# Optimization experiments

Hardware: AMD Instinct MI355X
Metric: run time of the kernel (lower is better)

Reference implementation:

```python
import jax, jax.numpy as jnp
import numpy as np

E = 4
K = 2
BN_EPS = 1e-3


def _silu(y):
    return y * jax.nn.sigmoid(y)


def _bn_silu_nchw(y, g, b, m, v):
    # eval-mode BatchNorm2d over channel axis of [B, C, H, W], then SiLU
    scale = (g / jnp.sqrt(v + BN_EPS))[None, :, None, None]
    shift = (b - m * g / jnp.sqrt(v + BN_EPS))[None, :, None, None]
    return _silu(y * scale + shift)


def setup_inputs() -> dict:
    key = jax.random.key(0)
    ks = jax.random.split(key, 20)
    B, C1, C2, H, W = 32, 256, 256, 80, 80
    c_ = C2 // 2  # 128
    s = 0.05
    return {
        "x": jax.random.normal(ks[0], (B, C1, H, W), jnp.float32),
        "w1": jax.random.normal(ks[1], (c_, C1), jnp.float32) * s,
        "bn1_g": jax.random.uniform(ks[2], (c_,), jnp.float32, 0.5, 1.5),
        "bn1_b": jax.random.normal(ks[3], (c_,), jnp.float32) * s,
        "bn1_m": jax.random.normal(ks[4], (c_,), jnp.float32) * s,
        "bn1_v": jax.random.uniform(ks[5], (c_,), jnp.float32, 0.5, 1.5),
        "router_w": jax.random.normal(ks[6], (E, c_), jnp.float32) * s,
        "router_b": jax.random.normal(ks[7], (E,), jnp.float32) * s,
        "ew": jax.random.normal(ks[8], (E, c_, c_, 3, 3), jnp.float32) * s,
        "ebn_g": jax.random.uniform(ks[9], (E, c_), jnp.float32, 0.5, 1.5),
        "ebn_b": jax.random.normal(ks[10], (E, c_), jnp.float32) * s,
        "ebn_m": jax.random.normal(ks[11], (E, c_), jnp.float32) * s,
        "ebn_v": jax.random.uniform(ks[12], (E, c_), jnp.float32, 0.5, 1.5),
        "w3": jax.random.normal(ks[13], (C2, c_), jnp.float32) * s,
        "bn3_g": jax.random.uniform(ks[14], (C2,), jnp.float32, 0.5, 1.5),
        "bn3_b": jax.random.normal(ks[15], (C2,), jnp.float32) * s,
        "bn3_m": jax.random.normal(ks[16], (C2,), jnp.float32) * s,
        "bn3_v": jax.random.uniform(ks[17], (C2,), jnp.float32, 0.5, 1.5),
    }


def reference(x, w1, bn1_g, bn1_b, bn1_m, bn1_v, router_w, router_b,
              ew, ebn_g, ebn_b, ebn_m, ebn_v, w3, bn3_g, bn3_b, bn3_m, bn3_v):
    B, C1, H, W = x.shape
    c_ = w1.shape[0]

    # conv1: 1x1 conv + BN + SiLU -> [B, c_, H, W]
    x_in = _bn_silu_nchw(jnp.einsum('bchw,oc->bohw', x, w1), bn1_g, bn1_b, bn1_m, bn1_v)

    # flatten pixels to tokens [N, c_] (N = B*H*W), matching permute(0,2,3,1).reshape
    tokens = x_in.transpose(0, 2, 3, 1).reshape(-1, c_)
    N = tokens.shape[0]

    # router: 1x1 conv with bias -> per-token logits [N, E]
    logits = tokens @ router_w.T + router_b
    probs = jax.nn.softmax(logits, axis=-1)

    topw, topi = jax.lax.top_k(probs, K)                  # [N, K]
    topw = topw / jnp.sum(topw, axis=-1, keepdims=True)

    # dense [N, E] combine weights: normalized top-k weight where selected, else 0
    wd = jnp.zeros((N, E), tokens.dtype).at[jnp.arange(N)[:, None], topi].set(topw)

    # experts: 3x3 conv applied to 1x1 patches with pad=1 -> only center tap matters
    center = ew[:, :, :, 1, 1]                            # [E, c_out, c_in]
    ye = jnp.einsum('nc,eoc->neo', tokens, center)        # [N, E, c_]
    inv = ebn_g / jnp.sqrt(ebn_v + BN_EPS)                # [E, c_]
    ye = _silu(ye * inv[None] + (ebn_b - ebn_m * inv)[None])

    out_moe = jnp.einsum('neo,ne->no', ye, wd)            # weighted scatter-add
    out_moe = out_moe.reshape(B, H, W, c_).transpose(0, 3, 1, 2)

    # conv3: 1x1 conv + BN + SiLU -> [B, C2, H, W]
    x_out = _bn_silu_nchw(jnp.einsum('bchw,oc->bohw', out_moe, w3), bn3_g, bn3_b, bn3_m, bn3_v)

    # shortcut (c1 == c2 here)
    return x_out + x
```

## Files before the change

### kernel.cpp

```cpp
#include <hip/hip_runtime.h>
#include <cstdint>
#include <cstddef>

#define NEXP 4
#define CH   128
#define C1   256
#define C2   256
#define HWSZ 6400
#define NTOKS 204800
#define BNE  1e-3f

using f32x4 = __attribute__((ext_vector_type(4))) float;
using f16x8 = __attribute__((ext_vector_type(8))) _Float16;
using s16x8 = __attribute__((ext_vector_type(8))) short;

static __device__ __forceinline__ unsigned short f2bf(float f) {
    union { float f; unsigned u; } v; v.f = f;
    unsigned r = v.u + 0x7fffu + ((v.u >> 16) & 1u);
    return (unsigned short)(r >> 16);
}
static __device__ __forceinline__ f32x4 zero4() {
    f32x4 z; z[0] = 0.f; z[1] = 0.f; z[2] = 0.f; z[3] = 0.f; return z;
}

#define ASWZ(row) ((((row) >> 1) & 3) << 3)

__global__ __launch_bounds__(256) void k0_pack(const float* __restrict__ ew,
                                               const float* __restrict__ w1,
                                               const float* __restrict__ w3,
                                               unsigned short* __restrict__ cen,
                                               _Float16* __restrict__ w1s,
                                               unsigned short* __restrict__ w3p) {
    int bid = blockIdx.x;
    int tid = threadIdx.x;
    if (bid < 256) {
        int idx = bid * 256 + tid;
        cen[idx] = f2bf(ew[(size_t)idx * 9 + 4]);
    } else if (bid < 384) {
        int lin = (bid - 256) * 256 + tid;
        int o = lin >> 8, k = lin & 255;
        int s = k >> 5, kk = k & 31;
        int kks = kk ^ ASWZ(o);
        float v = w1[o * C1 + k];
        _Float16 h = (_Float16)v;
        w1s[((s * 2 + 0) * 128 + o) * 32 + kks] = h;
        w1s[((s * 2 + 1) * 128 + o) * 32 + kks] = (_Float16)((v - (float)h) * 2048.0f);
    } else {
        int lin = (bid - 384) * 256 + tid;
        int o = lin >> 7, k = lin & 127;
        int s = k >> 5, kk = k & 31;
        int kks = kk ^ ASWZ(o);
        w3p[(s * 256 + o) * 32 + kks] = f2bf(w3[o * CH + k]);
    }
}

__global__ __launch_bounds__(256, 4) void k1_conv1_router(
    const float* __restrict__ x, const _Float16* __restrict__ w1s,
    const float* __restrict__ bn1_g, const float* __restrict__ bn1_b,
    const float* __restrict__ bn1_m, const float* __restrict__ bn1_v,
    const float* __restrict__ rw, const float* __restrict__ rb,
    unsigned short* __restrict__ tokens, float* __restrict__ wd)
{
    const int tid  = threadIdx.x;
    const int lane = tid & 63;
    const int n15  = lane & 15;
    const int quad = lane >> 4;
    const int wv   = tid >> 6;

    const int nt0 = blockIdx.x * 64;
    const int b   = nt0 / HWSZ;
    const int hw0 = nt0 % HWSZ;

    __shared__ union {
        struct { _Float16 Bh[64 * 72]; _Float16 Bl[64 * 72]; } s;
        struct { float tok[64 * 132]; float logit[64 * 4]; } e;
    } u;
    __shared__ float s1_l[128], t1_l[128];

    if (tid < 128) {
        float s = bn1_g[tid] / sqrtf(bn1_v[tid] + BNE);
        s1_l[tid] = s;
        t1_l[tid] = bn1_b[tid] - bn1_m[tid] * s;
    }

    f32x4 acc_m[2][4], acc_c[2][4];
    #pragma unroll
    for (int i = 0; i < 2; i++)
        #pragma unroll
        for (int j = 0; j < 4; j++) { acc_m[i][j] = zero4(); acc_c[i][j] = zero4(); }

    for (int S = 0; S < 4; S++) {
        {
            int i  = tid & 63;
            int kg = tid >> 6;
            #pragma unroll
            for (int r = 0; r < 4; r++) {
                int k4 = kg * 16 + r * 4;
                const float* xp = x + ((size_t)(b * C1 + S * 64 + k4)) * HWSZ + hw0 + i;
                float v0 = xp[0], v1 = xp[HWSZ], v2 = xp[2 * HWSZ], v3 = xp[3 * HWSZ];
                _Float16* bh = &u.s.Bh[i * 72 + k4];
                _Float16* bl = &u.s.Bl[i * 72 + k4];
                _Float16 h0 = (_Float16)v0, h1 = (_Float16)v1, h2 = (_Float16)v2, h3 = (_Float16)v3;
                bh[0] = h0; bh[1] = h1; bh[2] = h2; bh[3] = h3;
                bl[0] = (_Float16)((v0 - (float)h0) * 2048.0f);
                bl[1] = (_Float16)((v1 - (float)h1) * 2048.0f);
                bl[2] = (_Float16)((v2 - (float)h2) * 2048.0f);
                bl[3] = (_Float16)((v3 - (float)h3) * 2048.0f);
            }
        }
        __syncthreads();

        #pragma unroll
        for (int kh = 0; kh < 2; kh++) {
            const int sl = S * 2 + kh;
            f16x8 a_h[2], a_l[2];
            #pragma unroll
            for (int mt = 0; mt < 2; mt++) {
                int row = (wv * 2 + mt) * 16 + n15;
                int col = (quad * 8) ^ ASWZ(row);
                a_h[mt] = *(const f16x8*)&w1s[((sl * 2 + 0) * 128 + row) * 32 + col];
                a_l[mt] = *(const f16x8*)&w1s[((sl * 2 + 1) * 128 + row) * 32 + col];
            }
            #pragma unroll
            for (int nt = 0; nt < 4; nt++) {
                int row = nt * 16 + n15;
                f16x8 b_h = *(const f16x8*)&u.s.Bh[row * 72 + kh * 32 + quad * 8];
                f16x8 b_l = *(const f16x8*)&u.s.Bl[row * 72 + kh * 32 + quad * 8];
                #pragma unroll
                for (int mt = 0; mt < 2; mt++) {
                    acc_m[mt][nt] = __builtin_amdgcn_mfma_f32_16x16x32_f16(a_h[mt], b_h, acc_m[mt][nt], 0, 0, 0);
                    acc_c[mt][nt] = __builtin_amdgcn_mfma_f32_16x16x32_f16(a_l[mt], b_h, acc_c[mt][nt], 0, 0, 0);
                    acc_c[mt][nt] = __builtin_amdgcn_mfma_f32_16x16x32_f16(a_h[mt], b_l, acc_c[mt][nt], 0, 0, 0);
                }
            }
        }
        __syncthreads();
    }

    #pragma unroll
    for (int mt = 0; mt < 2; mt++)
        #pragma unroll
        for (int nt = 0; nt < 4; nt++)
            #pragma unroll
            for (int r = 0; r < 4; r++) {
                int o  = (wv * 2 + mt) * 16 + quad * 4 + r;
                int tk = nt * 16 + n15;
                float y1 = acc_m[mt][nt][r] + acc_c[mt][nt][r] * (1.0f / 2048.0f);
                float y  = y1 * s1_l[o] + t1_l[o];
                u.e.tok[tk * 132 + o] = y / (1.0f + __expf(-y));
            }
    __syncthreads();

    {
        int tk = tid >> 2;
        int e  = tid & 3;
        const float* trow = &u.e.tok[tk * 132];
        const float* wrow = &rw[e * CH];
        float a0 = 0.f, a1 = 0.f, a2 = 0.f, a3 = 0.f;
        #pragma unroll 8
        for (int c = 0; c < CH; c += 4) {
            a0 = fmaf(trow[c + 0], wrow[c + 0], a0);
            a1 = fmaf(trow[c + 1], wrow[c + 1], a1);
            a2 = fmaf(trow[c + 2], wrow[c + 2], a2);
            a3 = fmaf(trow[c + 3], wrow[c + 3], a3);
        }
        u.e.logit[tk * 4 + e] = ((a0 + a1) + (a2 + a3)) + rb[e];
    }
    __syncthreads();

    if (tid < 64) {
        const float* lg = &u.e.logit[tid * 4];
        float l0 = lg[0], l1 = lg[1], l2 = lg[2], l3 = lg[3];
        int i1 = 0; float m1 = l0;
        if (l1 > m1) { m1 = l1; i1 = 1; }
        if (l2 > m1) { m1 = l2; i1 = 2; }
        if (l3 > m1) { m1 = l3; i1 = 3; }
        int i2 = -1; float m2 = -3.4e38f;
        if (i1 != 0 && l0 > m2) { m2 = l0; i2 = 0; }
        if (i1 != 1 && l1 > m2) { m2 = l1; i2 = 1; }
        if (i1 != 2 && l2 > m2) { m2 = l2; i2 = 2; }
        if (i1 != 3 && l3 > m2) { m2 = l3; i2 = 3; }
        float p2 = __expf(m2 - m1);
        float wa = 1.0f / (1.0f + p2);
        float wb = p2 * wa;
        float4 wout;
        wout.x = (i1 == 0) ? wa : ((i2 == 0) ? wb : 0.0f);
        wout.y = (i1 == 1) ? wa : ((i2 == 1) ? wb : 0.0f);
        wout.z = (i1 == 2) ? wa : ((i2 == 2) ? wb : 0.0f);
        wout.w = (i1 == 3) ? wa : ((i2 == 3) ? wb : 0.0f);
        *(float4*)&wd[(size_t)(nt0 + tid) * 4] = wout;
    }

    #pragma unroll
    for (int rep = 0; rep < 8; rep++) {
        int lin = rep * 256 + tid;
        int n   = lin >> 5;
        int c4  = (lin & 31) * 4;
        const float* tp = &u.e.tok[n * 132 + c4];
        ushort4 pk;
        pk.x = f2bf(tp[0]); pk.y = f2bf(tp[1]); pk.z = f2bf(tp[2]); pk.w = f2bf(tp[3]);
        *(ushort4*)&tokens[(size_t)(nt0 + n) * CH + c4] = pk;
    }
}

__global__ __launch_bounds__(256, 2) void k2_experts(
    const unsigned short* __restrict__ tokens, const unsigned short* __restrict__ cen,
    const float* __restrict__ wd,
    const float* __restrict__ ebn_g, const float* __restrict__ ebn_b,
    const float* __restrict__ ebn_m, const float* __restrict__ ebn_v,
    unsigned short* __restrict__ moe)
{
    const int tid  = threadIdx.x;
    const int lane = tid & 63;
    const int wv   = tid >> 6;
    const int n15  = lane & 15;
    const int quad = lane >> 4;
    const int qm   = wv & 1;
    const int qn   = wv >> 1;
    const int nt0  = blockIdx.x * 128;

    __shared__ unsigned short Bt[128 * 136];
    __shared__ float wd_l[512];
    __shared__ float inv_l[512], sh_l[512];

    #pragma unroll
    for (int rep = 0; rep < 8; rep++) {
        int lin = rep * 256 + tid;
        int n   = lin >> 4;
        int c8  = (lin & 15) * 8;
        *(uint4*)&Bt[n * 136 + c8] = *(const uint4*)&tokens[(size_t)(nt0 + n) * CH + c8];
    }
    wd_l[tid]       = wd[(size_t)nt0 * 4 + tid];
    wd_l[256 + tid] = wd[(size_t)nt0 * 4 + 256 + tid];
    #pragma unroll
    for (int r = 0; r < 2; r++) {
        int idx = r * 256 + tid;
        float iv = ebn_g[idx] / sqrtf(ebn_v[idx] + BNE);
        inv_l[idx] = iv;
        sh_l[idx]  = ebn_b[idx] - ebn_m[idx] * iv;
    }

    f32x4 oacc[4][4];
    #pragma unroll
    for (int i = 0; i < 4; i++)
        #pragma unroll
        for (int j = 0; j < 4; j++) oacc[i][j] = zero4();

    __syncthreads();

    for (int e = 0; e < NEXP; e++) {
        s16x8 a[4][4];
        #pragma unroll
        for (int kk = 0; kk < 4; kk++)
            #pragma unroll
            for (int i = 0; i < 4; i++)
                a[kk][i] = *(const s16x8*)&cen[((size_t)e * CH + qm * 64 + i * 16 + n15) * CH + kk * 32 + quad * 8];

        f32x4 acc[4][4];
        #pragma unroll
        for (int i = 0; i < 4; i++)
            #pragma unroll
            for (int j = 0; j < 4; j++) acc[i][j] = zero4();

        #pragma unroll
        for (int kk = 0; kk < 4; kk++) {
            int ko = kk * 32 + quad * 8;
            s16x8 bb[4];
            #pragma unroll
            for (int i = 0; i < 4; i++)
                bb[i] = *(const s16x8*)&Bt[(qn * 64 + i * 16 + n15) * 136 + ko];
            #pragma unroll
            for (int mt = 0; mt < 4; mt++)
                #pragma unroll
                for (int nt = 0; nt < 4; nt++)
                    acc[mt][nt] = __builtin_amdgcn_mfma_f32_16x16x32_bf16(a[kk][mt], bb[nt], acc[mt][nt], 0, 0, 0);
        }

        #pragma unroll
        for (int mt = 0; mt < 4; mt++)
            #pragma unroll
            for (int nt = 0; nt < 4; nt++) {
                float wde = wd_l[(qn * 64 + nt * 16 + n15) * 4 + e];
                #pragma unroll
                for (int r = 0; r < 4; r++) {
                    int o = qm * 64 + mt * 16 + quad * 4 + r;
                    float y = acc[mt][nt][r] * inv_l[e * CH + o] + sh_l[e * CH + o];
                    oacc[mt][nt][r] += wde * (y / (1.0f + __expf(-y)));
                }
            }
    }

    #pragma unroll
    for (int mt = 0; mt < 4; mt++)
        #pragma unroll
        for (int nt = 0; nt < 4; nt++) {
            int tk = qn * 64 + nt * 16 + n15;
            int ob = qm * 64 + mt * 16 + quad * 4;
            ushort4 pk;
            pk.x = f2bf(oacc[mt][nt][0]); pk.y = f2bf(oacc[mt][nt][1]);
            pk.z = f2bf(oacc[mt][nt][2]); pk.w = f2bf(oacc[mt][nt][3]);
            *(ushort4*)&moe[(size_t)(nt0 + tk) * CH + ob] = pk;
        }
}

__global__ __launch_bounds__(256, 3) void k3_conv3(
    const unsigned short* __restrict__ moe, const unsigned short* __restrict__ w3p,
    const float* __restrict__ bn3_g, const float* __restrict__ bn3_b,
    const float* __restrict__ bn3_m, const float* __restrict__ bn3_v,
    const float* __restrict__ x, float* __restrict__ out)
{
    const int tid  = threadIdx.x;
    const int lane = tid & 63;
    const int wv   = tid >> 6;
    const int n15  = lane & 15;
    const int quad = lane >> 4;
    const int nt0  = blockIdx.x * 64;
    const int b    = nt0 / HWSZ;
    const int hw0  = nt0 % HWSZ;

    __shared__ union {
        unsigned short B3[64 * 136];
        float scr[128 * 68];
    } u;
    __shared__ float s3_l[256], t3_l[256];

    {
        float s = bn3_g[tid] / sqrtf(bn3_v[tid] + BNE);
        s3_l[tid] = s;
        t3_l[tid] = bn3_b[tid] - bn3_m[tid] * s;
    }

    #pragma unroll
    for (int rep = 0; rep < 2; rep++) {
        int lin = rep * 256 + tid;
        int n   = lin >> 3;
        int c16 = (lin & 7) * 16;
        *(uint4*)&u.B3[n * 136 + c16]     = *(const uint4*)&moe[(size_t)(nt0 + n) * CH + c16];
        *(uint4*)&u.B3[n * 136 + c16 + 8] = *(const uint4*)&moe[(size_t)(nt0 + n) * CH + c16 + 8];
    }

    f32x4 acc[4][4];
    #pragma unroll
    for (int i = 0; i < 4; i++)
        #pragma unroll
        for (int j = 0; j < 4; j++) acc[i][j] = zero4();

    __syncthreads();

    for (int s = 0; s < 4; s++) {
        s16x8 af[4];
        #pragma unroll
        for (int mt = 0; mt < 4; mt++) {
            int row = (wv * 4 + mt) * 16 + n15;
            int col = (quad * 8) ^ ASWZ(row);
            af[mt] = *(const s16x8*)&w3p[(s * 256 + row) * 32 + col];
        }
        s16x8 bf[4];
        #pragma unroll
        for (int nt = 0; nt < 4; nt++)
            bf[nt] = *(const s16x8*)&u.B3[(nt * 16 + n15) * 136 + s * 32 + quad * 8];
        #pragma unroll
        for (int mt = 0; mt < 4; mt++)
            #pragma unroll
            for (int nt = 0; nt < 4; nt++)
                acc[mt][nt] = __builtin_amdgcn_mfma_f32_16x16x32_bf16(af[mt], bf[nt], acc[mt][nt], 0, 0, 0);
    }

    #pragma unroll
    for (int h = 0; h < 2; h++) {
        __syncthreads();
        if ((wv >> 1) == h) {
            int wvl = wv & 1;
            #pragma unroll
            for (int mt = 0; mt < 4; mt++)
                #pragma unroll
                for (int nt = 0; nt < 4; nt++) {
                    int tk = nt * 16 + n15;
                    #pragma unroll
                    for (int r = 0; r < 4; r++) {
                        int o_l = wvl * 64 + mt * 16 + quad * 4 + r;
                        int o2  = h * 128 + o_l;
                        float y = acc[mt][nt][r] * s3_l[o2] + t3_l[o2];
                        u.scr[o_l * 68 + tk] = y / (1.0f + __expf(-y));
                    }
                }
        }
        __syncthreads();
        #pragma unroll
        for (int rep = 0; rep < 8; rep++) {
            int lin = rep * 256 + tid;
            int row = lin >> 4;
            int t4  = (lin & 15) * 4;
            int o2  = h * 128 + row;
            size_t g = ((size_t)(b * C2 + o2)) * HWSZ + hw0 + t4;
            f32x4 v = *(const f32x4*)&u.scr[row * 68 + t4];
            const float4 xs = *(const float4*)&x[g];
            float4 w;
            w.x = v[0] + xs.x; w.y = v[1] + xs.y; w.z = v[2] + xs.z; w.w = v[3] + xs.w;
            *(float4*)&out[g] = w;
        }
    }
}

extern "C" void kernel_launch(void* const* d_in, const int* in_sizes, int n_in,
                              void* d_out, int out_size, void* d_ws, size_t ws_size,
                              hipStream_t stream) {
    const float* x     = (const float*)d_in[0];
    const float* w1    = (const float*)d_in[1];
    const float* bn1_g = (const float*)d_in[2];
    const float* bn1_b = (const float*)d_in[3];
    const float* bn1_m = (const float*)d_in[4];
    const float* bn1_v = (const float*)d_in[5];
    const float* rw    = (const float*)d_in[6];
    const float* rb    = (const float*)d_in[7];
    const float* ew    = (const float*)d_in[8];
    const float* ebn_g = (const float*)d_in[9];
    const float* ebn_b = (const float*)d_in[10];
    const float* ebn_m = (const float*)d_in[11];
    const float* ebn_v = (const float*)d_in[12];
    const float* w3    = (const float*)d_in[13];
    const float* bn3_g = (const float*)d_in[14];
    const float* bn3_b = (const float*)d_in[15];
    const float* bn3_m = (const float*)d_in[16];
    const float* bn3_v = (const float*)d_in[17];
    float* out = (float*)d_out;

    char* ws = (char*)d_ws;
    unsigned short* tokens = (unsigned short*)(ws);
    unsigned short* moe    = (unsigned short*)(ws + 52428800);
    float*          wdv    = (float*)(ws + 104857600);
    unsigned short* cen    = (unsigned short*)(ws + 108134400);
    _Float16*       w1s    = (_Float16*)(ws + 108265472);
    unsigned short* w3p    = (unsigned short*)(ws + 108396544);

    k0_pack<<<dim3(512), dim3(256), 0, stream>>>(ew, w1, w3, cen, w1s, w3p);
    k1_conv1_router<<<dim3(3200), dim3(256), 0, stream>>>(x, w1s, bn1_g, bn1_b, bn1_m, bn1_v,
                                                          rw, rb, tokens, wdv);
    k2_experts<<<dim3(1600), dim3(256), 0, stream>>>(tokens, cen, wdv,
                                                     ebn_g, ebn_b, ebn_m, ebn_v, moe);
    k3_conv3<<<dim3(3200), dim3(256), 0, stream>>>(moe, w3p, bn3_g, bn3_b, bn3_m, bn3_v, x, out);
    (void)in_sizes; (void)n_in; (void)out_size; (void)ws_size;
}
```

Before: 654.3 us.

## Pipeline x loads in conv1, shrink expert tiles, drop weight swizzle

In the conv1 kernel, the x tile is now register-prefetched one K-slice ahead into double-buffered LDS with a k-major layout, and the epilogue is split into two 32-token halves to shrink LDS use. The expert kernel moves to 64-token blocks with 4 waves each covering 32 output channels. It streams the expert weight fragments from global with register double-buffering, which raises occupancy from 2 to 4 blocks per SM. The XOR swizzle on global weight packing is removed. Together these aim to hide global load latency and improve occupancy, at the cost of more barriers and repeated weight fetches per block.

```diff
diff --git a/kernel.cpp b/kernel.cpp
--- a/kernel.cpp
+++ b/kernel.cpp
@@ -12,6 +12,7 @@
 
 using f32x4 = __attribute__((ext_vector_type(4))) float;
 using f16x8 = __attribute__((ext_vector_type(8))) _Float16;
+using f16x4 = __attribute__((ext_vector_type(4))) _Float16;
 using s16x8 = __attribute__((ext_vector_type(8))) short;
 
 static __device__ __forceinline__ unsigned short f2bf(float f) {
@@ -22,8 +23,6 @@
 static __device__ __forceinline__ f32x4 zero4() {
     f32x4 z; z[0] = 0.f; z[1] = 0.f; z[2] = 0.f; z[3] = 0.f; return z;
 }
-
-#define ASWZ(row) ((((row) >> 1) & 3) << 3)
 
 __global__ __launch_bounds__(256) void k0_pack(const float* __restrict__ ew,
                                                const float* __restrict__ w1,
@@ -40,17 +39,15 @@
         int lin = (bid - 256) * 256 + tid;
         int o = lin >> 8, k = lin & 255;
         int s = k >> 5, kk = k & 31;
-        int kks = kk ^ ASWZ(o);
         float v = w1[o * C1 + k];
         _Float16 h = (_Float16)v;
-        w1s[((s * 2 + 0) * 128 + o) * 32 + kks] = h;
-        w1s[((s * 2 + 1) * 128 + o) * 32 + kks] = (_Float16)((v - (float)h) * 2048.0f);
+        w1s[((s * 2 + 0) * 128 + o) * 32 + kk] = h;
+        w1s[((s * 2 + 1) * 128 + o) * 32 + kk] = (_Float16)((v - (float)h) * 2048.0f);
     } else {
         int lin = (bid - 384) * 256 + tid;
         int o = lin >> 7, k = lin & 127;
         int s = k >> 5, kk = k & 31;
-        int kks = kk ^ ASWZ(o);
-        w3p[(s * 256 + o) * 32 + kks] = f2bf(w3[o * CH + k]);
+        w3p[(s * 256 + o) * 32 + kk] = f2bf(w3[o * CH + k]);
     }
 }
 
@@ -72,8 +69,8 @@
     const int hw0 = nt0 % HWSZ;
 
     __shared__ union {
-        struct { _Float16 Bh[64 * 72]; _Float16 Bl[64 * 72]; } s;
-        struct { float tok[64 * 132]; float logit[64 * 4]; } e;
+        struct { _Float16 Bh[2][2048]; _Float16 Bl[2][2048]; } s;
+        struct { float tokh[32 * 132]; float logit[128]; } e;
     } u;
     __shared__ float s1_l[128], t1_l[128];
 
@@ -89,121 +86,138 @@
         #pragma unroll
         for (int j = 0; j < 4; j++) { acc_m[i][j] = zero4(); acc_c[i][j] = zero4(); }
 
-    for (int S = 0; S < 4; S++) {
-        {
-            int i  = tid & 63;
-            int kg = tid >> 6;
-            #pragma unroll
-            for (int r = 0; r < 4; r++) {
-                int k4 = kg * 16 + r * 4;
-                const float* xp = x + ((size_t)(b * C1 + S * 64 + k4)) * HWSZ + hw0 + i;
-                float v0 = xp[0], v1 = xp[HWSZ], v2 = xp[2 * HWSZ], v3 = xp[3 * HWSZ];
-                _Float16* bh = &u.s.Bh[i * 72 + k4];
-                _Float16* bl = &u.s.Bl[i * 72 + k4];
-                _Float16 h0 = (_Float16)v0, h1 = (_Float16)v1, h2 = (_Float16)v2, h3 = (_Float16)v3;
-                bh[0] = h0; bh[1] = h1; bh[2] = h2; bh[3] = h3;
-                bl[0] = (_Float16)((v0 - (float)h0) * 2048.0f);
-                bl[1] = (_Float16)((v1 - (float)h1) * 2048.0f);
-                bl[2] = (_Float16)((v2 - (float)h2) * 2048.0f);
-                bl[3] = (_Float16)((v3 - (float)h3) * 2048.0f);
+    const int ti = tid & 63;
+    const int kg = tid >> 6;
+
+    float pf[2][8];
+
+    #pragma unroll
+    for (int r = 0; r < 2; r++) {
+        const float* xp = x + ((size_t)(b * C1 + 0 * 32 + kg * 8 + r * 4)) * HWSZ + hw0 + ti;
+        #pragma unroll
+        for (int j = 0; j < 4; j++) pf[0][r * 4 + j] = xp[(size_t)j * HWSZ];
+    }
+
+    #pragma unroll
+    for (int S = 0; S < 8; S++) {
+        const int pb = S & 1;
+        #pragma unroll
+        for (int r = 0; r < 2; r++) {
+            float v0 = pf[pb][r * 4 + 0], v1 = pf[pb][r * 4 + 1];
+            float v2 = pf[pb][r * 4 + 2], v3 = pf[pb][r * 4 + 3];
+            _Float16 h0 = (_Float16)v0, h1 = (_Float16)v1, h2 = (_Float16)v2, h3 = (_Float16)v3;
+            f16x4 hv; hv[0] = h0; hv[1] = h1; hv[2] = h2; hv[3] = h3;
+            f16x4 lv;
+            lv[0] = (_Float16)((v0 - (float)h0) * 2048.0f);
+            lv[1] = (_Float16)((v1 - (float)h1) * 2048.0f);
+            lv[2] = (_Float16)((v2 - (float)h2) * 2048.0f);
+            lv[3] = (_Float16)((v3 - (float)h3) * 2048.0f);
+            *(f16x4*)&u.s.Bh[pb][(kg * 64 + ti) * 8 + r * 4] = hv;
+            *(f16x4*)&u.s.Bl[pb][(kg * 64 + ti) * 8 + r * 4] = lv;
+        }
+        __syncthreads();
+        if (S < 7) {
+            #pragma unroll
+            for (int r = 0; r < 2; r++) {
+                const float* xp = x + ((size_t)(b * C1 + (S + 1) * 32 + kg * 8 + r * 4)) * HWSZ + hw0 + ti;
+                #pragma unroll
+                for (int j = 0; j < 4; j++) pf[pb ^ 1][r * 4 + j] = xp[(size_t)j * HWSZ];
             }
         }
-        __syncthreads();
-
-        #pragma unroll
-        for (int kh = 0; kh < 2; kh++) {
-            const int sl = S * 2 + kh;
-            f16x8 a_h[2], a_l[2];
+        f16x8 a_h[2], a_l[2];
+        #pragma unroll
+        for (int mt = 0; mt < 2; mt++) {
+            int row = (wv * 2 + mt) * 16 + n15;
+            a_h[mt] = *(const f16x8*)&w1s[((S * 2 + 0) * 128 + row) * 32 + quad * 8];
+            a_l[mt] = *(const f16x8*)&w1s[((S * 2 + 1) * 128 + row) * 32 + quad * 8];
+        }
+        #pragma unroll
+        for (int nt = 0; nt < 4; nt++) {
+            f16x8 b_h = *(const f16x8*)&u.s.Bh[pb][(quad * 64 + nt * 16 + n15) * 8];
+            f16x8 b_l = *(const f16x8*)&u.s.Bl[pb][(quad * 64 + nt * 16 + n15) * 8];
             #pragma unroll
             for (int mt = 0; mt < 2; mt++) {
-                int row = (wv * 2 + mt) * 16 + n15;
-                int col = (quad * 8) ^ ASWZ(row);
-                a_h[mt] = *(const f16x8*)&w1s[((sl * 2 + 0) * 128 + row) * 32 + col];
-                a_l[mt] = *(const f16x8*)&w1s[((sl * 2 + 1) * 128 + row) * 32 + col];
+                acc_m[mt][nt] = __builtin_amdgcn_mfma_f32_16x16x32_f16(a_h[mt], b_h, acc_m[mt][nt], 0, 0, 0);
+                acc_c[mt][nt] = __builtin_amdgcn_mfma_f32_16x16x32_f16(a_l[mt], b_h, acc_c[mt][nt], 0, 0, 0);
+                acc_c[mt][nt] = __builtin_amdgcn_mfma_f32_16x16x32_f16(a_h[mt], b_l, acc_c[mt][nt], 0, 0, 0);
             }
-            #pragma unroll
-            for (int nt = 0; nt < 4; nt++) {
-                int row = nt * 16 + n15;
-                f16x8 b_h = *(const f16x8*)&u.s.Bh[row * 72 + kh * 32 + quad * 8];
-                f16x8 b_l = *(const f16x8*)&u.s.Bl[row * 72 + kh * 32 + quad * 8];
+        }
+    }
+    __syncthreads();
+
+    #pragma unroll
+    for (int h = 0; h < 2; h++) {
+        if (h) __syncthreads();
+        #pragma unroll
+        for (int mt = 0; mt < 2; mt++)
+            #pragma unroll
+            for (int nt2 = 0; nt2 < 2; nt2++) {
+                int nt = h * 2 + nt2;
                 #pragma unroll
-                for (int mt = 0; mt < 2; mt++) {
-                    acc_m[mt][nt] = __builtin_amdgcn_mfma_f32_16x16x32_f16(a_h[mt], b_h, acc_m[mt][nt], 0, 0, 0);
-                    acc_c[mt][nt] = __builtin_amdgcn_mfma_f32_16x16x32_f16(a_l[mt], b_h, acc_c[mt][nt], 0, 0, 0);
-                    acc_c[mt][nt] = __builtin_amdgcn_mfma_f32_16x16x32_f16(a_h[mt], b_l, acc_c[mt][nt], 0, 0, 0);
+                for (int r = 0; r < 4; r++) {
+                    int o  = (wv * 2 + mt) * 16 + quad * 4 + r;
+                    int tk = nt2 * 16 + n15;
+                    float y1 = acc_m[mt][nt][r] + acc_c[mt][nt][r] * (1.0f / 2048.0f);
+                    float y  = y1 * s1_l[o] + t1_l[o];
+                    u.e.tokh[tk * 132 + o] = y / (1.0f + __expf(-y));
                 }
             }
-        }
         __syncthreads();
-    }
-
-    #pragma unroll
-    for (int mt = 0; mt < 2; mt++)
-        #pragma unroll
-        for (int nt = 0; nt < 4; nt++)
-            #pragma unroll
-            for (int r = 0; r < 4; r++) {
-                int o  = (wv * 2 + mt) * 16 + quad * 4 + r;
-                int tk = nt * 16 + n15;
-                float y1 = acc_m[mt][nt][r] + acc_c[mt][nt][r] * (1.0f / 2048.0f);
-                float y  = y1 * s1_l[o] + t1_l[o];
-                u.e.tok[tk * 132 + o] = y / (1.0f + __expf(-y));
+
+        if (tid < 128) {
+            int tk = tid >> 2;
+            int e  = tid & 3;
+            const float* trow = &u.e.tokh[tk * 132];
+            const float* wrow = &rw[e * CH];
+            float a0 = 0.f, a1 = 0.f, a2 = 0.f, a3 = 0.f;
+            #pragma unroll 8
+            for (int c = 0; c < CH; c += 4) {
+                a0 = fmaf(trow[c + 0], wrow[c + 0], a0);
+                a1 = fmaf(trow[c + 1], wrow[c + 1], a1);
+                a2 = fmaf(trow[c + 2], wrow[c + 2], a2);
+                a3 = fmaf(trow[c + 3], wrow[c + 3], a3);
             }
-    __syncthreads();
-
-    {
-        int tk = tid >> 2;
-        int e  = tid & 3;
-        const float* trow = &u.e.tok[tk * 132];
-        const float* wrow = &rw[e * CH];
-        float a0 = 0.f, a1 = 0.f, a2 = 0.f, a3 = 0.f;
-        #pragma unroll 8
-        for (int c = 0; c < CH; c += 4) {
-            a0 = fmaf(trow[c + 0], wrow[c + 0], a0);
-            a1 = fmaf(trow[c + 1], wrow[c + 1], a1);
-            a2 = fmaf(trow[c + 2], wrow[c + 2], a2);
-            a3 = fmaf(trow[c + 3], wrow[c + 3], a3);
-        }
-        u.e.logit[tk * 4 + e] = ((a0 + a1) + (a2 + a3)) + rb[e];
-    }
-    __syncthreads();
-
-    if (tid < 64) {
-        const float* lg = &u.e.logit[tid * 4];
-        float l0 = lg[0], l1 = lg[1], l2 = lg[2], l3 = lg[3];
-        int i1 = 0; float m1 = l0;
-        if (l1 > m1) { m1 = l1; i1 = 1; }
-        if (l2 > m1) { m1 = l2; i1 = 2; }
-        if (l3 > m1) { m1 = l3; i1 = 3; }
-        int i2 = -1; float m2 = -3.4e38f;
-        if (i1 != 0 && l0 > m2) { m2 = l0; i2 = 0; }
-        if (i1 != 1 && l1 > m2) { m2 = l1; i2 = 1; }
-        if (i1 != 2 && l2 > m2) { m2 = l2; i2 = 2; }
-        if (i1 != 3 && l3 > m2) { m2 = l3; i2 = 3; }
-        float p2 = __expf(m2 - m1);
-        float wa = 1.0f / (1.0f + p2);
-        float wb = p2 * wa;
-        float4 wout;
-        wout.x = (i1 == 0) ? wa : ((i2 == 0) ? wb : 0.0f);
-        wout.y = (i1 == 1) ? wa : ((i2 == 1) ? wb : 0.0f);
-        wout.z = (i1 == 2) ? wa : ((i2 == 2) ? wb : 0.0f);
-        wout.w = (i1 == 3) ? wa : ((i2 == 3) ? wb : 0.0f);
-        *(float4*)&wd[(size_t)(nt0 + tid) * 4] = wout;
-    }
-
-    #pragma unroll
-    for (int rep = 0; rep < 8; rep++) {
-        int lin = rep * 256 + tid;
-        int n   = lin >> 5;
-        int c4  = (lin & 31) * 4;
-        const float* tp = &u.e.tok[n * 132 + c4];
-        ushort4 pk;
-        pk.x = f2bf(tp[0]); pk.y = f2bf(tp[1]); pk.z = f2bf(tp[2]); pk.w = f2bf(tp[3]);
-        *(ushort4*)&tokens[(size_t)(nt0 + n) * CH + c4] = pk;
-    }
-}
-
-__global__ __launch_bounds__(256, 2) void k2_experts(
+            u.e.logit[tk * 4 + e] = ((a0 + a1) + (a2 + a3)) + rb[e];
+        }
+        __syncthreads();
+
+        if (tid < 32) {
+            const float* lg = &u.e.logit[tid * 4];
+            float l0 = lg[0], l1 = lg[1], l2 = lg[2], l3 = lg[3];
+            int i1 = 0; float m1 = l0;
+            if (l1 > m1) { m1 = l1; i1 = 1; }
+            if (l2 > m1) { m1 = l2; i1 = 2; }
+            if (l3 > m1) { m1 = l3; i1 = 3; }
+            int i2 = -1; float m2 = -3.4e38f;
+            if (i1 != 0 && l0 > m2) { m2 = l0; i2 = 0; }
+            if (i1 != 1 && l1 > m2) { m2 = l1; i2 = 1; }
+            if (i1 != 2 && l2 > m2) { m2 = l2; i2 = 2; }
+            if (i1 != 3 && l3 > m2) { m2 = l3; i2 = 3; }
+            float p2 = __expf(m2 - m1);
+            float wa = 1.0f / (1.0f + p2);
+            float wb = p2 * wa;
+            float4 wout;
+            wout.x = (i1 == 0) ? wa : ((i2 == 0) ? wb : 0.0f);
+            wout.y = (i1 == 1) ? wa : ((i2 == 1) ? wb : 0.0f);
+            wout.z = (i1 == 2) ? wa : ((i2 == 2) ? wb : 0.0f);
+            wout.w = (i1 == 3) ? wa : ((i2 == 3) ? wb : 0.0f);
+            *(float4*)&wd[(size_t)(nt0 + h * 32 + tid) * 4] = wout;
+        }
+
+        #pragma unroll
+        for (int rep = 0; rep < 4; rep++) {
+            int lin = rep * 256 + tid;
+            int n   = lin >> 5;
+            int c4  = (lin & 31) * 4;
+            const float* tp = &u.e.tokh[n * 132 + c4];
+            ushort4 pk;
+            pk.x = f2bf(tp[0]); pk.y = f2bf(tp[1]); pk.z = f2bf(tp[2]); pk.w = f2bf(tp[3]);
+            *(ushort4*)&tokens[(size_t)(nt0 + h * 32 + n) * CH + c4] = pk;
+        }
+    }
+}
+
+__global__ __launch_bounds__(256, 4) void k2_experts(
     const unsigned short* __restrict__ tokens, const unsigned short* __restrict__ cen,
     const float* __restrict__ wd,
     const float* __restrict__ ebn_g, const float* __restrict__ ebn_b,
@@ -215,23 +229,20 @@
     const int wv   = tid >> 6;
     const int n15  = lane & 15;
     const int quad = lane >> 4;
-    const int qm   = wv & 1;
-    const int qn   = wv >> 1;
-    const int nt0  = blockIdx.x * 128;
-
-    __shared__ unsigned short Bt[128 * 136];
-    __shared__ float wd_l[512];
+    const int nt0  = blockIdx.x * 64;
+
+    __shared__ unsigned short Bt[64 * 136];
+    __shared__ float wd_l[256];
     __shared__ float inv_l[512], sh_l[512];
 
     #pragma unroll
-    for (int rep = 0; rep < 8; rep++) {
+    for (int rep = 0; rep < 4; rep++) {
         int lin = rep * 256 + tid;
         int n   = lin >> 4;
         int c8  = (lin & 15) * 8;
         *(uint4*)&Bt[n * 136 + c8] = *(const uint4*)&tokens[(size_t)(nt0 + n) * CH + c8];
     }
-    wd_l[tid]       = wd[(size_t)nt0 * 4 + tid];
-    wd_l[256 + tid] = wd[(size_t)nt0 * 4 + 256 + tid];
+    wd_l[tid] = wd[(size_t)nt0 * 4 + tid];
     #pragma unroll
     for (int r = 0; r < 2; r++) {
         int idx = r * 256 + tid;
@@ -240,62 +251,63 @@
         sh_l[idx]  = ebn_b[idx] - ebn_m[idx] * iv;
     }
 
-    f32x4 oacc[4][4];
-    #pragma unroll
-    for (int i = 0; i < 4; i++)
-        #pragma unroll
-        for (int j = 0; j < 4; j++) oacc[i][j] = zero4();
+    f32x4 acc[2][4], oacc[2][4];
+    #pragma unroll
+    for (int i = 0; i < 2; i++)
+        #pragma unroll
+        for (int j = 0; j < 4; j++) { acc[i][j] = zero4(); oacc[i][j] = zero4(); }
+
+    s16x8 ap[2][2];
+    #pragma unroll
+    for (int mt = 0; mt < 2; mt++)
+        ap[0][mt] = *(const s16x8*)&cen[((size_t)(0 * CH) + wv * 32 + mt * 16 + n15) * CH + 0 * 32 + quad * 8];
 
     __syncthreads();
 
-    for (int e = 0; e < NEXP; e++) {
-        s16x8 a[4][4];
-        #pragma unroll
-        for (int kk = 0; kk < 4; kk++)
-            #pragma unroll
-            for (int i = 0; i < 4; i++)
-                a[kk][i] = *(const s16x8*)&cen[((size_t)e * CH + qm * 64 + i * 16 + n15) * CH + kk * 32 + quad * 8];
-
-        f32x4 acc[4][4];
-        #pragma unroll
-        for (int i = 0; i < 4; i++)
-            #pragma unroll
-            for (int j = 0; j < 4; j++) acc[i][j] = zero4();
-
-        #pragma unroll
-        for (int kk = 0; kk < 4; kk++) {
-            int ko = kk * 32 + quad * 8;
-            s16x8 bb[4];
-            #pragma unroll
-            for (int i = 0; i < 4; i++)
-                bb[i] = *(const s16x8*)&Bt[(qn * 64 + i * 16 + n15) * 136 + ko];
-            #pragma unroll
-            for (int mt = 0; mt < 4; mt++)
+    #pragma unroll
+    for (int ek = 0; ek < 16; ek++) {
+        const int e   = ek >> 2;
+        const int kk  = ek & 3;
+        const int cur = ek & 1;
+        if (ek < 15) {
+            const int en = (ek + 1) >> 2, kn = (ek + 1) & 3;
+            #pragma unroll
+            for (int mt = 0; mt < 2; mt++)
+                ap[cur ^ 1][mt] = *(const s16x8*)&cen[((size_t)(en * CH) + wv * 32 + mt * 16 + n15) * CH + kn * 32 + quad * 8];
+        }
+        s16x8 bb[4];
+        #pragma unroll
+        for (int nt = 0; nt < 4; nt++)
+            bb[nt] = *(const s16x8*)&Bt[(nt * 16 + n15) * 136 + kk * 32 + quad * 8];
+        #pragma unroll
+        for (int mt = 0; mt < 2; mt++)
+            #pragma unroll
+            for (int nt = 0; nt < 4; nt++)
+                acc[mt][nt] = __builtin_amdgcn_mfma_f32_16x16x32_bf16(ap[cur][mt], bb[nt], acc[mt][nt], 0, 0, 0);
+
+        if (kk == 3) {
+            #pragma unroll
+            for (int mt = 0; mt < 2; mt++)
                 #pragma unroll
-                for (int nt = 0; nt < 4; nt++)
-                    acc[mt][nt] = __builtin_amdgcn_mfma_f32_16x16x32_bf16(a[kk][mt], bb[nt], acc[mt][nt], 0, 0, 0);
-        }
-
-        #pragma unroll
-        for (int mt = 0; mt < 4; mt++)
-            #pragma unroll
-            for (int nt = 0; nt < 4; nt++) {
-                float wde = wd_l[(qn * 64 + nt * 16 + n15) * 4 + e];
-                #pragma unroll
-                for (int r = 0; r < 4; r++) {
-                    int o = qm * 64 + mt * 16 + quad * 4 + r;
-                    float y = acc[mt][nt][r] * inv_l[e * CH + o] + sh_l[e * CH + o];
-                    oacc[mt][nt][r] += wde * (y / (1.0f + __expf(-y)));
+                for (int nt = 0; nt < 4; nt++) {
+                    float wde = wd_l[(nt * 16 + n15) * 4 + e];
+                    #pragma unroll
+                    for (int r = 0; r < 4; r++) {
+                        int o = wv * 32 + mt * 16 + quad * 4 + r;
+                        float y = acc[mt][nt][r] * inv_l[e * CH + o] + sh_l[e * CH + o];
+                        oacc[mt][nt][r] += wde * (y / (1.0f + __expf(-y)));
+                    }
+                    acc[mt][nt] = zero4();
                 }
-            }
-    }
-
-    #pragma unroll
-    for (int mt = 0; mt < 4; mt++)
+        }
+    }
+
+    #pragma unroll
+    for (int mt = 0; mt < 2; mt++)
         #pragma unroll
         for (int nt = 0; nt < 4; nt++) {
-            int tk = qn * 64 + nt * 16 + n15;
-            int ob = qm * 64 + mt * 16 + quad * 4;
+            int tk = nt * 16 + n15;
+            int ob = wv * 32 + mt * 16 + quad * 4;
             ushort4 pk;
             pk.x = f2bf(oacc[mt][nt][0]); pk.y = f2bf(oacc[mt][nt][1]);
             pk.z = f2bf(oacc[mt][nt][2]); pk.w = f2bf(oacc[mt][nt][3]);
@@ -352,8 +364,7 @@
         #pragma unroll
         for (int mt = 0; mt < 4; mt++) {
             int row = (wv * 4 + mt) * 16 + n15;
-            int col = (quad * 8) ^ ASWZ(row);
-            af[mt] = *(const s16x8*)&w3p[(s * 256 + row) * 32 + col];
+            af[mt] = *(const s16x8*)&w3p[(s * 256 + row) * 32 + quad * 8];
         }
         s16x8 bf[4];
         #pragma unroll
@@ -436,7 +447,7 @@
     k0_pack<<<dim3(512), dim3(256), 0, stream>>>(ew, w1, w3, cen, w1s, w3p);
     k1_conv1_router<<<dim3(3200), dim3(256), 0, stream>>>(x, w1s, bn1_g, bn1_b, bn1_m, bn1_v,
                                                           rw, rb, tokens, wdv);
-    k2_experts<<<dim3(1600), dim3(256), 0, stream>>>(tokens, cen, wdv,
+    k2_experts<<<dim3(3200), dim3(256), 0, stream>>>(tokens, cen, wdv,
                                                      ebn_g, ebn_b, ebn_m, ebn_v, moe);
     k3_conv3<<<dim3(3200), dim3(256), 0, stream>>>(moe, w3p, bn3_g, bn3_b, bn3_m, bn3_v, x, out);
     (void)in_sizes; (void)n_in; (void)out_size; (void)ws_size;
```

After: 824.4 us. 1.26x slower.
